# Performance work log

Measured on AMD Instinct MI355X. Metric: run time of the kernel, lower is better.

The kernel has to match this reference:

```python
import jax, jax.numpy as jnp
import numpy as np

N, D, E, K, L, NF, VOCAB = 100000, 128, 600000, 3, 3, 9, 100
BN_EPS = 1e-5
S = 0.05


def setup_inputs() -> dict:
    key = jax.random.key(0)
    ks = jax.random.split(key, 8)
    return {
        "x": jax.random.randint(ks[0], (N, NF), 0, VOCAB),
        "k_edges": jax.random.randint(ks[1], (K, 2, E), 0, N),
        "emb_tables": jax.random.normal(ks[2], (NF, VOCAB, D), jnp.float32) * S,
        "W1": jax.random.normal(ks[3], (L, D, 2 * D), jnp.float32) * S,
        "b1": jnp.zeros((L, 2 * D), jnp.float32),
        "g1": jnp.ones((L, 2 * D), jnp.float32),
        "be1": jnp.zeros((L, 2 * D), jnp.float32),
        "W2": jax.random.normal(ks[4], (L, 2 * D, D), jnp.float32) * S,
        "b2": jnp.zeros((L, D), jnp.float32),
        "eps": jnp.zeros((L,), jnp.float32),
        "alpha": jnp.zeros((L, K), jnp.float32),
        "bn_g": jnp.ones((L, D), jnp.float32),
        "bn_b": jnp.zeros((L, D), jnp.float32),
    }


def _bn(h, g, b):
    # training-mode BatchNorm1d over the node (batch) axis
    mu = h.mean(axis=0)
    var = h.var(axis=0)
    return (h - mu) * jax.lax.rsqrt(var + BN_EPS) * g + b


def _gin(h, src, dst, eps_l, W1_l, b1_l, g1_l, be1_l, W2_l, b2_l):
    # NodeGINConv (train_eps): mlp((1+eps)*x + sum_{j->i} x_j)
    agg = jax.ops.segment_sum(h[src], dst, num_segments=N)  # [N, D]
    z = (1.0 + eps_l) * h + agg
    z = jax.nn.relu(_bn(z @ W1_l + b1_l, g1_l, be1_l))  # [N, 2D]
    return z @ W2_l + b2_l  # [N, D]


def reference(x, k_edges, emb_tables, W1, b1, g1, be1, W2, b2, eps, alpha, bn_g, bn_b):
    # AtomEncoder: sum of per-feature embedding lookups -> [N, D]
    h = jnp.take_along_axis(
        emb_tables.transpose(1, 0, 2),  # [VOCAB, NF, D]
        x.T[..., None].transpose(1, 0, 2) * 0 + 0,  # placeholder avoided below
        axis=0,
    ) if False else emb_tables[jnp.arange(NF)[None, :], x].sum(axis=1)
    for l in range(L):
        # one shared wrapped GIN conv applied to each of the K relational edge sets
        msgs = jax.vmap(
            lambda e: _gin(h, e[0], e[1], eps[l], W1[l], b1[l], g1[l], be1[l], W2[l], b2[l])
        )(k_edges)  # [K, N, D]
        a = jax.nn.softmax(alpha[l])  # [K]
        h = jnp.einsum('knd,k->nd', msgs, a)
        h = jax.nn.relu(_bn(h, bn_g[l], bn_b[l]))  # dropout p=0 / eval -> identity
    return h
```

## Files before the change

### kernel.cpp

```cpp
#include <hip/hip_runtime.h>

#define NV     100000
#define DD     128
#define D2     256
#define EE     600000
#define KK     3
#define LL     3
#define NFEAT  9
#define VOCABS 100

#define NBKT   196
#define BCAP   8192

typedef __attribute__((ext_vector_type(8))) short short8;
typedef __attribute__((ext_vector_type(4))) float f32x4;
typedef __attribute__((ext_vector_type(4))) unsigned int uint4v;

#define PA      0
#define PA2     8
#define PB2     136
#define PA1K(k) (264 + (k)*512)
#define PB1K(k) (264 + (k)*512 + 256)

#define ZS(k)  ((k)*512)
#define ZQ(k)  ((k)*512 + 256)
#define HSUM   1536
#define HSQ    1664

#define HB_OFF   ((size_t)0)
#define ZIN_OFF  ((size_t)25600000)
#define HNB_OFF  ((size_t)102400000)
#define O_BASE   ((size_t)128000000)

__device__ __forceinline__ unsigned short f2bf(float f) {
    union { float f; unsigned int u; } v; v.f = f;
    return (unsigned short)((v.u + 0x7FFFu + ((v.u >> 16) & 1u)) >> 16);
}
__device__ __forceinline__ float bf2f(unsigned short u) {
    union { unsigned int u; float f; } v; v.u = ((unsigned int)u) << 16;
    return v.f;
}

__global__ void k_embed(const int* __restrict__ x, const float* __restrict__ emb,
                        unsigned short* __restrict__ hb) {
    int id = blockIdx.x*256 + threadIdx.x;
    int n = id >> 5, q = id & 31;
    if (n >= NV) return;
    const int* xr = x + n*NFEAT;
    f32x4 acc = {0.f,0.f,0.f,0.f};
    #pragma unroll
    for (int f = 0; f < NFEAT; ++f) {
        int idx = xr[f];
        acc += *(const f32x4*)(emb + ((size_t)(f*VOCABS + idx)*DD + q*4));
    }
    unsigned short pk[4];
    pk[0] = f2bf(acc[0]); pk[1] = f2bf(acc[1]); pk[2] = f2bf(acc[2]); pk[3] = f2bf(acc[3]);
    *(unsigned long long*)(hb + (size_t)n*DD + q*4) = *(unsigned long long*)pk;
}

__global__ void kA_bin(const int* __restrict__ ke, int* __restrict__ cursor,
                       uint2* __restrict__ pairs) {
    __shared__ int hist[NBKT], excl[NBKT], ofs[NBKT], gbase[NBKT];
    __shared__ int sc[256];
    __shared__ uint2 buf[4096];
    const int rel = blockIdx.y, t = threadIdx.x;
    const int e0 = blockIdx.x * 4096;
    const int cnt = min(4096, EE - e0);
    const int* srcA = ke + (size_t)(rel*2)*EE + e0;
    const int* dstA = ke + (size_t)(rel*2+1)*EE + e0;
    if (t < NBKT) hist[t] = 0;
    __syncthreads();
    for (int i = t; i < cnt; i += 256) atomicAdd(&hist[dstA[i] >> 9], 1);
    __syncthreads();
    const int hv = (t < NBKT) ? hist[t] : 0;
    sc[t] = hv;
    for (int off = 1; off < 256; off <<= 1) {
        __syncthreads();
        int v = (t >= off) ? sc[t-off] : 0;
        __syncthreads();
        sc[t] += v;
    }
    __syncthreads();
    if (t < NBKT) {
        excl[t] = sc[t] - hv;
        ofs[t]  = sc[t] - hv;
        if (hv > 0) gbase[t] = atomicAdd(&cursor[rel*NBKT + t], hv);
    }
    __syncthreads();
    for (int i = t; i < cnt; i += 256) {
        unsigned int s = (unsigned int)srcA[i], d = (unsigned int)dstA[i];
        int p = atomicAdd(&ofs[d >> 9], 1);
        uint2 u; u.x = s; u.y = d;
        buf[p] = u;
    }
    __syncthreads();
    for (int i = t; i < cnt; i += 256) {
        uint2 u = buf[i];
        int b = (int)(u.y >> 9);
        int pos = gbase[b] + (i - excl[b]);
        if (pos < BCAP) pairs[(size_t)(rel*NBKT + b)*BCAP + pos] = u;
    }
}

__global__ void kB_scan(const int* __restrict__ cursor, int* __restrict__ ebase) {
    __shared__ int sc[256];
    const int t = threadIdx.x;
    for (int rel = 0; rel < KK; ++rel) {
        int hv = (t < NBKT) ? min(cursor[rel*NBKT + t], BCAP) : 0;
        sc[t] = hv;
        for (int off = 1; off < 256; off <<= 1) {
            __syncthreads();
            int v = (t >= off) ? sc[t-off] : 0;
            __syncthreads();
            sc[t] += v;
        }
        __syncthreads();
        if (t < NBKT) ebase[rel*NBKT + t] = sc[t] - hv;
        __syncthreads();
    }
}

__global__ void kB_fill(const uint2* __restrict__ pairs, const int* __restrict__ cursor,
                        const int* __restrict__ ebase, int* __restrict__ rp,
                        int* __restrict__ col) {
    __shared__ int h2[512], excl[512], cur[512], sc[256];
    const int b = blockIdx.x, rel = blockIdx.y, t = threadIdx.x;
    const int lo = b * 512;
    const int cnt = min(cursor[rel*NBKT + b], BCAP);
    const int base = ebase[rel*NBKT + b];
    const uint2* P = pairs + (size_t)(rel*NBKT + b)*BCAP;
    h2[t] = 0; h2[t+256] = 0; cur[t] = 0; cur[t+256] = 0;
    __syncthreads();
    for (int i = t; i < cnt; i += 256) atomicAdd(&h2[(int)P[i].y - lo], 1);
    __syncthreads();
    const int a0 = h2[2*t], a1 = h2[2*t+1];
    sc[t] = a0 + a1;
    for (int off = 1; off < 256; off <<= 1) {
        __syncthreads();
        int v = (t >= off) ? sc[t-off] : 0;
        __syncthreads();
        sc[t] += v;
    }
    __syncthreads();
    const int e2 = sc[t] - (a0 + a1);
    excl[2*t] = e2; excl[2*t+1] = e2 + a0;
    __syncthreads();
    for (int tt = t; tt < 512; tt += 256) {
        int n = lo + tt;
        if (n <= NV) rp[(size_t)rel*(NV+1) + n] = base + excl[tt];
    }
    for (int i = t; i < cnt; i += 256) {
        uint2 u = P[i];
        int r = (int)u.y - lo;
        int p = atomicAdd(&cur[r], 1);
        col[(size_t)rel*EE + base + excl[r] + p] = (int)u.x;
    }
}

__global__ void k_prep(const float* __restrict__ W1, const float* __restrict__ W2,
                       const float* __restrict__ alpha, const int l,
                       unsigned short* __restrict__ w1f, unsigned short* __restrict__ w2f,
                       float* __restrict__ params) {
    int id = blockIdx.x*256 + threadIdx.x;
    if (id == 0) {
        float a0 = alpha[l*KK+0], a1 = alpha[l*KK+1], a2 = alpha[l*KK+2];
        float m = fmaxf(a0, fmaxf(a1, a2));
        float e0 = expf(a0-m), e1 = expf(a1-m), e2 = expf(a2-m);
        float inv = 1.f/(e0+e1+e2);
        params[PA+0] = e0*inv; params[PA+1] = e1*inv; params[PA+2] = e2*inv;
    }
    if (id < 4096) {
        int kt = id >> 10, nt = (id >> 6) & 15, lane = id & 63;
        int r = lane & 15, g = lane >> 4;
        const float* Wl = W1 + (size_t)l*DD*D2;
        #pragma unroll
        for (int e = 0; e < 8; ++e) {
            int kk = kt*32 + g*8 + e, c = nt*16 + r;
            w1f[(size_t)id*8 + e] = f2bf(Wl[(size_t)kk*D2 + c]);
        }
    } else if (id < 8192) {
        int id2 = id - 4096;
        int kt = id2 >> 9, nt = (id2 >> 6) & 7, lane = id2 & 63;
        int r = lane & 15, g = lane >> 4;
        const float* Wl = W2 + (size_t)l*D2*DD;
        #pragma unroll
        for (int e = 0; e < 8; ++e) {
            int kk = kt*32 + g*8 + e, c = nt*16 + r;
            w2f[(size_t)id2*8 + e] = f2bf(Wl[(size_t)kk*DD + c]);
        }
    }
}

__global__ void k_gather3(const unsigned short* __restrict__ hb, const int* __restrict__ rp,
                          const int* __restrict__ col, const float* __restrict__ epsp,
                          unsigned short* __restrict__ zin) {
    int gid = blockIdx.x*256 + threadIdx.x;
    int n = gid >> 6;
    if (n >= NV) return;
    const int lane = threadIdx.x & 63;
    const int q = lane >> 4, r = lane & 15;
    const uint4v* h4 = (const uint4v*)hb;
    const float epsv = 1.0f + epsp[0];
    const uint4v sv = h4[(size_t)n*16 + r];
    int b0[KK], dg[KK], cv[KK];
    #pragma unroll
    for (int k = 0; k < KK; ++k) {
        const int* rpk = rp + (size_t)k*(NV+1) + n;
        int a = rpk[0], b = rpk[1];
        b0[k] = a; dg[k] = b - a;
        cv[k] = (lane < dg[k]) ? col[(size_t)k*EE + a + lane] : 0;
    }
    float acc[KK][8];
    #pragma unroll
    for (int k = 0; k < KK; ++k)
        #pragma unroll
        for (int i = 0; i < 8; ++i) acc[k][i] = 0.0f;
    #pragma unroll
    for (int k = 0; k < KK; ++k) {
        const int dc = min(dg[k], 64);
        for (int base = 0; base < dc; base += 8) {
            const int e0 = base + q;
            const int e1 = base + q + 4;
            int s0 = __shfl(cv[k], e0);
            int s1 = __shfl(cv[k], e1);
            uint4v v0 = h4[(size_t)s0*16 + r];
            uint4v v1 = h4[(size_t)s1*16 + r];
            if (e0 < dc) {
                #pragma unroll
                for (int c = 0; c < 4; ++c) {
                    acc[k][2*c]   += bf2f((unsigned short)(v0[c] & 0xFFFFu));
                    acc[k][2*c+1] += bf2f((unsigned short)(v0[c] >> 16));
                }
            }
            if (e1 < dc) {
                #pragma unroll
                for (int c = 0; c < 4; ++c) {
                    acc[k][2*c]   += bf2f((unsigned short)(v1[c] & 0xFFFFu));
                    acc[k][2*c+1] += bf2f((unsigned short)(v1[c] >> 16));
                }
            }
        }
        for (int j = b0[k] + 64 + q; j < b0[k] + dg[k]; j += 4) {
            int s0 = col[(size_t)k*EE + j];
            uint4v v0 = h4[(size_t)s0*16 + r];
            #pragma unroll
            for (int c = 0; c < 4; ++c) {
                acc[k][2*c]   += bf2f((unsigned short)(v0[c] & 0xFFFFu));
                acc[k][2*c+1] += bf2f((unsigned short)(v0[c] >> 16));
            }
        }
    }
    #pragma unroll
    for (int k = 0; k < KK; ++k) {
        #pragma unroll
        for (int i = 0; i < 8; ++i) {
            acc[k][i] += __shfl_xor(acc[k][i], 16);
            acc[k][i] += __shfl_xor(acc[k][i], 32);
        }
        if (q == 0) {
            uint4v pk;
            #pragma unroll
            for (int c = 0; c < 4; ++c) {
                float lo = acc[k][2*c]   + epsv * bf2f((unsigned short)(sv[c] & 0xFFFFu));
                float hi = acc[k][2*c+1] + epsv * bf2f((unsigned short)(sv[c] >> 16));
                pk[c] = (unsigned int)f2bf(lo) | ((unsigned int)f2bf(hi) << 16);
            }
            ((uint4v*)(zin + (size_t)k*NV*DD))[(size_t)n*16 + r] = pk;
        }
    }
}

__launch_bounds__(256, 2)
__global__ void k_stats3(const unsigned short* __restrict__ zin,
                         const unsigned short* __restrict__ w1f,
                         float* __restrict__ stats) {
    __shared__ __align__(16) unsigned short bfr1[32768];
    __shared__ float scf[1024];
    const int t = threadIdx.x;
    const int krel = blockIdx.y;
    const unsigned short* zk = zin + (size_t)krel*NV*DD;
    float* zsum = stats + ZS(krel);
    float* zsq  = stats + ZQ(krel);
    for (int i = t; i < 4096; i += 256)
        *(uint4v*)(bfr1 + i*8) = *(const uint4v*)(w1f + i*8);
    const int lane = t & 63, w = t >> 6;
    const int r_ = lane & 15, g = lane >> 4;
    const int rt = w & 1, ch = w >> 1;
    __syncthreads();
    float ssum[8] = {0,0,0,0,0,0,0,0};
    float ssq[8]  = {0,0,0,0,0,0,0,0};
    for (int tile = blockIdx.x; tile < NV/32; tile += gridDim.x) {
        const int row0 = tile*32;
        short8 af[4];
        #pragma unroll
        for (int kt = 0; kt < 4; ++kt)
            af[kt] = *(const short8*)(zk + (size_t)(row0 + rt*16 + r_)*DD + kt*32 + g*8);
        #pragma unroll
        for (int ct = 0; ct < 8; ++ct) {
            const int ntg = ch*8 + ct;
            f32x4 c = {0.f,0.f,0.f,0.f};
            #pragma unroll
            for (int kt = 0; kt < 4; ++kt) {
                short8 b = *(const short8*)(bfr1 + ((size_t)((kt*16 + ntg)*64 + lane))*8);
                c = __builtin_amdgcn_mfma_f32_16x16x32_bf16(af[kt], b, c, 0, 0, 0);
            }
            float s = c[0]+c[1]+c[2]+c[3];
            float q = c[0]*c[0]+c[1]*c[1]+c[2]*c[2]+c[3]*c[3];
            s += __shfl_xor(s, 16); q += __shfl_xor(q, 16);
            s += __shfl_xor(s, 32); q += __shfl_xor(q, 32);
            ssum[ct] += s; ssq[ct] += q;
        }
    }
    if (g == 0) {
        #pragma unroll
        for (int ct = 0; ct < 8; ++ct) {
            const int colc = (ch*8 + ct)*16 + r_;
            scf[rt*256 + colc]       = ssum[ct];
            scf[512 + rt*256 + colc] = ssq[ct];
        }
    }
    __syncthreads();
    atomicAdd(zsum + t, scf[t]       + scf[256 + t]);
    atomicAdd(zsq  + t, scf[512 + t] + scf[768 + t]);
}

__global__ void k_bnprep3(float* __restrict__ stats,
                          const float* __restrict__ g1l, const float* __restrict__ be1l,
                          float* __restrict__ params) {
    int j = threadIdx.x;
    #pragma unroll
    for (int k = 0; k < KK; ++k) {
        float ak  = params[PA + k];
        float mu  = stats[ZS(k) + j] * (1.0f/NV);
        float var = stats[ZQ(k) + j] * (1.0f/NV) - mu*mu;
        float A = g1l[j] * rsqrtf(var + 1e-5f);
        params[PA1K(k) + j] = ak * A;
        params[PB1K(k) + j] = ak * (be1l[j] - mu*A);
        stats[ZS(k) + j] = 0.0f; stats[ZQ(k) + j] = 0.0f;
    }
}

#define LOAD_AF(AF, TILE) {                                                        \
    const int rowp_ = (TILE)*32;                                                   \
    _Pragma("unroll")                                                              \
    for (int k = 0; k < KK; ++k) {                                                 \
        _Pragma("unroll")                                                          \
        for (int kt = 0; kt < 4; ++kt)                                             \
            AF[k][kt] = *(const short8*)(zin + (size_t)k*NV*DD                     \
                          + (size_t)(rowp_ + rt*16 + r_)*DD + kt*32 + g*8);        \
    }                                                                              \
}

#define GBODY(AF, AFN) {                                                           \
    const int cur_ = tile, nx_ = tile + step;                                      \
    f32x4 y[4];                                                                    \
    _Pragma("unroll")                                                              \
    for (int ct = 0; ct < 4; ++ct) y[ct] = (f32x4){0.f,0.f,0.f,0.f};               \
    _Pragma("unroll")                                                              \
    for (int k = 0; k < KK; ++k) {                                                 \
        _Pragma("unroll")                                                          \
        for (int ct = 0; ct < 4; ++ct) {                                           \
            const int ntg = ch*4 + ct;                                             \
            f32x4 c = {0.f,0.f,0.f,0.f};                                           \
            _Pragma("unroll")                                                      \
            for (int kt = 0; kt < 4; ++kt) {                                       \
                short8 b = *(const short8*)(bfr1 + ((size_t)((kt*16 + ntg)*64 + lane))*8); \
                c = __builtin_amdgcn_mfma_f32_16x16x32_bf16(AF[k][kt], b, c, 0, 0, 0); \
            }                                                                      \
            _Pragma("unroll")                                                      \
            for (int reg = 0; reg < 4; ++reg)                                      \
                y[ct][reg] += fmaxf(pa1[k][ct]*c[reg] + pb1[k][ct], 0.0f);         \
        }                                                                          \
    }                                                                              \
    if (nx_ < NT) LOAD_AF(AFN, nx_);                                               \
    __syncthreads();                                                               \
    _Pragma("unroll")                                                              \
    for (int ct = 0; ct < 4; ++ct) {                                               \
        const int col2 = ((ch*4 + ct)*16 + r_)*2;                                  \
        _Pragma("unroll")                                                          \
        for (int reg = 0; reg < 4; ++reg) {                                        \
            const int row = rt*16 + g*4 + reg;                                     \
            *(unsigned short*)(yt + row*512 + (col2 ^ ((row & 15) << 4))) = f2bf(y[ct][reg]); \
        }                                                                          \
    }                                                                              \
    __syncthreads();                                                               \
    short8 ya[8];                                                                  \
    _Pragma("unroll")                                                              \
    for (int kt = 0; kt < 8; ++kt)                                                 \
        ya[kt] = *(const short8*)(yt + arow*512 + ((kt*64 + g*16) ^ ((arow & 15) << 4))); \
    _Pragma("unroll")                                                              \
    for (int ct2 = 0; ct2 < 2; ++ct2) {                                            \
        const int ntg2 = ch*2 + ct2;                                               \
        f32x4 c = {0.f,0.f,0.f,0.f};                                               \
        _Pragma("unroll")                                                          \
        for (int kt = 0; kt < 8; ++kt) {                                           \
            short8 b = *(const short8*)(bfr2 + ((size_t)((kt*8 + ntg2)*64 + lane))*8); \
            c = __builtin_amdgcn_mfma_f32_16x16x32_bf16(ya[kt], b, c, 0, 0, 0);    \
        }                                                                          \
        unsigned short* hp = hnb + (size_t)(cur_*32 + rt*16 + g*4)*DD + ntg2*16 + r_; \
        float ps = 0.0f, pq = 0.0f;                                                \
        _Pragma("unroll")                                                          \
        for (int reg = 0; reg < 4; ++reg) {                                        \
            float xv = c[reg];                                                     \
            hp[(size_t)reg*DD] = f2bf(xv);                                         \
            ps += xv; pq += xv*xv;                                                 \
        }                                                                          \
        ps += __shfl_xor(ps, 16); pq += __shfl_xor(pq, 16);                        \
        ps += __shfl_xor(ps, 32); pq += __shfl_xor(pq, 32);                        \
        ssum[ct2] += ps; ssq[ct2] += pq;                                           \
    }                                                                              \
    tile = nx_;                                                                    \
}

__launch_bounds__(512, 2)
__global__ void k_gemm2f(const unsigned short* __restrict__ zin,
                         const unsigned short* __restrict__ w1f,
                         const unsigned short* __restrict__ w2f,
                         const float* __restrict__ params,
                         unsigned short* __restrict__ hnb,
                         float* __restrict__ hsum, float* __restrict__ hsq) {
    __shared__ __align__(16) unsigned short bfr1[32768];
    __shared__ __align__(16) unsigned short bfr2[32768];
    __shared__ __align__(16) unsigned char yt[16384];
    const int t = threadIdx.x;
    for (int i = t; i < 4096; i += 512)
        *(uint4v*)(bfr1 + i*8) = *(const uint4v*)(w1f + i*8);
    for (int i = t; i < 4096; i += 512)
        *(uint4v*)(bfr2 + i*8) = *(const uint4v*)(w2f + i*8);
    const int lane = t & 63, w = t >> 6;
    const int r_ = lane & 15, g = lane >> 4;
    const int rt = w & 1, ch = w >> 1;
    const int arow = rt*16 + r_;
    float pa1[KK][4], pb1[KK][4];
    #pragma unroll
    for (int k = 0; k < KK; ++k) {
        #pragma unroll
        for (int ct = 0; ct < 4; ++ct) {
            const int colc = (ch*4 + ct)*16 + r_;
            pa1[k][ct] = params[PA1K(k) + colc];
            pb1[k][ct] = params[PB1K(k) + colc];
        }
    }
    __syncthreads();
    float ssum[2] = {0,0}, ssq[2] = {0,0};
    const int NT = NV/32;
    const int step = gridDim.x;
    int tile = blockIdx.x;
    short8 afA[KK][4], afB[KK][4];
    LOAD_AF(afA, tile);
    while (tile < NT) {
        GBODY(afA, afB);
        if (tile >= NT) break;
        GBODY(afB, afA);
    }
    __syncthreads();
    float* scf = (float*)yt;
    if (g == 0) {
        #pragma unroll
        for (int ct2 = 0; ct2 < 2; ++ct2) {
            scf[w*32 + ct2*16 + r_]       = ssum[ct2];
            scf[256 + w*32 + ct2*16 + r_] = ssq[ct2];
        }
    }
    __syncthreads();
    if (t < 128) {
        const int chc = t >> 5, idx = t & 31;
        float s = 0.0f, q = 0.0f;
        #pragma unroll
        for (int rr = 0; rr < 2; ++rr) {
            s += scf[(chc*2 + rr)*32 + idx];
            q += scf[256 + (chc*2 + rr)*32 + idx];
        }
        atomicAdd(hsum + t, s);
        atomicAdd(hsq + t, q);
    }
}

__global__ void k_bnprep2(float* __restrict__ hsum, float* __restrict__ hsq,
                          const float* __restrict__ bng, const float* __restrict__ bnb,
                          float* __restrict__ params) {
    int j = threadIdx.x;
    float mu  = hsum[j] * (1.0f/NV);
    float var = hsq[j]  * (1.0f/NV) - mu*mu;
    float A = bng[j] * rsqrtf(var + 1e-5f);
    params[PA2 + j] = A;
    params[PB2 + j] = bnb[j] - mu*A;
    hsum[j] = 0.0f; hsq[j] = 0.0f;
}

__global__ void k_bnapply_mid(const unsigned short* __restrict__ hnb,
                              const float* __restrict__ params,
                              unsigned short* __restrict__ hb) {
    int id = blockIdx.x*256 + threadIdx.x;
    const int col0 = (id & 15)*8;
    short8 v = *(const short8*)(hnb + (size_t)id*8);
    f32x4 A0 = *(const f32x4*)(params + PA2 + col0);
    f32x4 A1 = *(const f32x4*)(params + PA2 + col0 + 4);
    f32x4 B0 = *(const f32x4*)(params + PB2 + col0);
    f32x4 B1 = *(const f32x4*)(params + PB2 + col0 + 4);
    short8 o;
    #pragma unroll
    for (int j = 0; j < 4; ++j) {
        o[j]   = (short)f2bf(fmaxf(A0[j]*bf2f((unsigned short)v[j])   + B0[j], 0.0f));
        o[j+4] = (short)f2bf(fmaxf(A1[j]*bf2f((unsigned short)v[j+4]) + B1[j], 0.0f));
    }
    *(short8*)(hb + (size_t)id*8) = o;
}

__global__ void k_bnapply_fin(const unsigned short* __restrict__ hnb,
                              const float* __restrict__ params,
                              float* __restrict__ out) {
    int id = blockIdx.x*256 + threadIdx.x;
    const int col0 = (id & 15)*8;
    short8 v = *(const short8*)(hnb + (size_t)id*8);
    f32x4 A0 = *(const f32x4*)(params + PA2 + col0);
    f32x4 A1 = *(const f32x4*)(params + PA2 + col0 + 4);
    f32x4 B0 = *(const f32x4*)(params + PB2 + col0);
    f32x4 B1 = *(const f32x4*)(params + PB2 + col0 + 4);
    f32x4 o0, o1;
    #pragma unroll
    for (int j = 0; j < 4; ++j) {
        o0[j] = fmaxf(A0[j]*bf2f((unsigned short)v[j])   + B0[j], 0.0f);
        o1[j] = fmaxf(A1[j]*bf2f((unsigned short)v[j+4]) + B1[j], 0.0f);
    }
    *(f32x4*)(out + (size_t)id*8)     = o0;
    *(f32x4*)(out + (size_t)id*8 + 4) = o1;
}

extern "C" void kernel_launch(void* const* d_in, const int* in_sizes, int n_in,
                              void* d_out, int out_size, void* d_ws, size_t ws_size,
                              hipStream_t stream) {
    const int*   x     = (const int*)d_in[0];
    const int*   ke    = (const int*)d_in[1];
    const float* emb   = (const float*)d_in[2];
    const float* W1    = (const float*)d_in[3];
    const float* g1    = (const float*)d_in[5];
    const float* be1   = (const float*)d_in[6];
    const float* W2    = (const float*)d_in[7];
    const float* eps   = (const float*)d_in[9];
    const float* alpha = (const float*)d_in[10];
    const float* bng   = (const float*)d_in[11];
    const float* bnb   = (const float*)d_in[12];

    char* ws = (char*)d_ws;
    unsigned short* hb     = (unsigned short*)(ws + HB_OFF);
    unsigned short* zin    = (unsigned short*)(ws + ZIN_OFF);
    unsigned short* hnb    = (unsigned short*)(ws + HNB_OFF);
    size_t o = O_BASE;
    unsigned short* w1f    = (unsigned short*)(ws + o);          o += 65536;
    unsigned short* w2f    = (unsigned short*)(ws + o);          o += 65536;
    float*          stats  = (float*)(ws + o);                   o += 8192;
    float*          params = (float*)(ws + o);                   o += 8192;
    int*            rp     = (int*)(ws + o);                     o += 1200128;
    int*            col    = (int*)(ws + o);                     o += 7200000;
    int*            cur    = (int*)(ws + o);                     o += 4096;
    int*            ebase  = (int*)(ws + o);                     o += 4096;
    uint2*          pairs  = (uint2*)(ws + ZIN_OFF);

    k_embed<<<12500, 256, 0, stream>>>(x, emb, hb);

    hipMemsetAsync(cur, 0, KK*NBKT*sizeof(int), stream);
    hipMemsetAsync(stats, 0, 8192, stream);
    kA_bin<<<dim3(147, KK), 256, 0, stream>>>(ke, cur, pairs);
    kB_scan<<<1, 256, 0, stream>>>(cur, ebase);
    kB_fill<<<dim3(NBKT, KK), 256, 0, stream>>>(pairs, cur, ebase, rp, col);

    for (int l = 0; l < LL; ++l) {
        k_prep<<<32, 256, 0, stream>>>(W1, W2, alpha, l, w1f, w2f, params);
        k_gather3<<<25000, 256, 0, stream>>>(hb, rp, col, eps + l, zin);
        k_stats3<<<dim3(512, KK), 256, 0, stream>>>(zin, w1f, stats);
        k_bnprep3<<<1, 256, 0, stream>>>(stats, g1 + l*D2, be1 + l*D2, params);
        k_gemm2f<<<256, 512, 0, stream>>>(zin, w1f, w2f, params, hnb,
                                          stats + HSUM, stats + HSQ);
        k_bnprep2<<<1, 128, 0, stream>>>(stats + HSUM, stats + HSQ,
                                         bng + l*DD, bnb + l*DD, params);
        if (l < LL-1) k_bnapply_mid<<<6250, 256, 0, stream>>>(hnb, params, hb);
        else          k_bnapply_fin<<<6250, 256, 0, stream>>>(hnb, params, (float*)d_out);
    }
}
```

Measured before the change: 720.9 us.

## Use zero sentinel row to drop gather bounds checks and double-buffer GEMM LDS

A zeroed padding row is added past the last node in the bf16 feature buffer, and out-of-range neighbor slots now point at it. This lets the gather loop drop its per-edge validity branches and accumulate unconditionally with packed bf16 unpacking and a hardware pack-convert instruction. The fused GEMM kernel ping-pongs between two LDS staging buffers, which removes one __syncthreads per tile. The cost is extra loads of the sentinel row for low-degree nodes, more workspace, and higher LDS use per block.

```diff
diff --git a/kernel.cpp b/kernel.cpp
--- a/kernel.cpp
+++ b/kernel.cpp
@@ -14,6 +14,7 @@
 
 typedef __attribute__((ext_vector_type(8))) short short8;
 typedef __attribute__((ext_vector_type(4))) float f32x4;
+typedef __attribute__((ext_vector_type(2))) float f32x2;
 typedef __attribute__((ext_vector_type(4))) unsigned int uint4v;
 
 #define PA      0
@@ -28,9 +29,9 @@
 #define HSQ    1664
 
 #define HB_OFF   ((size_t)0)
-#define ZIN_OFF  ((size_t)25600000)
-#define HNB_OFF  ((size_t)102400000)
-#define O_BASE   ((size_t)128000000)
+#define ZIN_OFF  ((size_t)25700000)
+#define HNB_OFF  ((size_t)102500000)
+#define O_BASE   ((size_t)128100000)
 
 __device__ __forceinline__ unsigned short f2bf(float f) {
     union { float f; unsigned int u; } v; v.f = f;
@@ -39,13 +40,22 @@
 __device__ __forceinline__ float bf2f(unsigned short u) {
     union { unsigned int u; float f; } v; v.u = ((unsigned int)u) << 16;
     return v.f;
+}
+__device__ __forceinline__ f32x2 up2(unsigned int v) {
+    union { unsigned int u[2]; f32x2 f; } w;
+    w.u[0] = v << 16;
+    w.u[1] = v & 0xFFFF0000u;
+    return w.f;
 }
 
 __global__ void k_embed(const int* __restrict__ x, const float* __restrict__ emb,
                         unsigned short* __restrict__ hb) {
     int id = blockIdx.x*256 + threadIdx.x;
     int n = id >> 5, q = id & 31;
-    if (n >= NV) return;
+    if (n >= NV) {
+        if (n < NV + 8) *(unsigned long long*)(hb + (size_t)n*DD + q*4) = 0ull;
+        return;
+    }
     const int* xr = x + n*NFEAT;
     f32x4 acc = {0.f,0.f,0.f,0.f};
     #pragma unroll
@@ -195,77 +205,73 @@
                           const int* __restrict__ col, const float* __restrict__ epsp,
                           unsigned short* __restrict__ zin) {
     int gid = blockIdx.x*256 + threadIdx.x;
-    int n = gid >> 6;
-    if (n >= NV) return;
+    int n0 = gid >> 6;
+    if (n0 >= NV) return;
+    const int n = __builtin_amdgcn_readfirstlane(n0);
     const int lane = threadIdx.x & 63;
     const int q = lane >> 4, r = lane & 15;
-    const uint4v* h4 = (const uint4v*)hb;
+    const int r16 = r << 4;
+    const char* hbase = (const char*)hb;
     const float epsv = 1.0f + epsp[0];
-    const uint4v sv = h4[(size_t)n*16 + r];
+    const uint4v sv = *(const uint4v*)(hbase + (((unsigned)n << 8) + r16));
     int b0[KK], dg[KK], cv[KK];
     #pragma unroll
     for (int k = 0; k < KK; ++k) {
-        const int* rpk = rp + (size_t)k*(NV+1) + n;
-        int a = rpk[0], b = rpk[1];
+        int a = rp[k*(NV+1) + n];
+        int b = rp[k*(NV+1) + n + 1];
         b0[k] = a; dg[k] = b - a;
-        cv[k] = (lane < dg[k]) ? col[(size_t)k*EE + a + lane] : 0;
-    }
-    float acc[KK][8];
+        cv[k] = (lane < dg[k]) ? col[(size_t)k*EE + a + lane] : NV;
+    }
+    f32x2 acc[KK][4];
     #pragma unroll
     for (int k = 0; k < KK; ++k)
         #pragma unroll
-        for (int i = 0; i < 8; ++i) acc[k][i] = 0.0f;
+        for (int c = 0; c < 4; ++c) acc[k][c] = (f32x2){0.f, 0.f};
     #pragma unroll
     for (int k = 0; k < KK; ++k) {
         const int dc = min(dg[k], 64);
         for (int base = 0; base < dc; base += 8) {
-            const int e0 = base + q;
-            const int e1 = base + q + 4;
-            int s0 = __shfl(cv[k], e0);
-            int s1 = __shfl(cv[k], e1);
-            uint4v v0 = h4[(size_t)s0*16 + r];
-            uint4v v1 = h4[(size_t)s1*16 + r];
-            if (e0 < dc) {
-                #pragma unroll
-                for (int c = 0; c < 4; ++c) {
-                    acc[k][2*c]   += bf2f((unsigned short)(v0[c] & 0xFFFFu));
-                    acc[k][2*c+1] += bf2f((unsigned short)(v0[c] >> 16));
-                }
-            }
-            if (e1 < dc) {
-                #pragma unroll
-                for (int c = 0; c < 4; ++c) {
-                    acc[k][2*c]   += bf2f((unsigned short)(v1[c] & 0xFFFFu));
-                    acc[k][2*c+1] += bf2f((unsigned short)(v1[c] >> 16));
-                }
+            int s0 = __shfl(cv[k], base + q);
+            int s1 = __shfl(cv[k], base + q + 4);
+            uint4v v0 = *(const uint4v*)(hbase + (((unsigned)s0 << 8) + r16));
+            uint4v v1 = *(const uint4v*)(hbase + (((unsigned)s1 << 8) + r16));
+            #pragma unroll
+            for (int c = 0; c < 4; ++c) {
+                acc[k][c] += up2(v0[c]);
+                acc[k][c] += up2(v1[c]);
             }
         }
         for (int j = b0[k] + 64 + q; j < b0[k] + dg[k]; j += 4) {
             int s0 = col[(size_t)k*EE + j];
-            uint4v v0 = h4[(size_t)s0*16 + r];
+            uint4v v0 = *(const uint4v*)(hbase + (((unsigned)s0 << 8) + r16));
             #pragma unroll
-            for (int c = 0; c < 4; ++c) {
-                acc[k][2*c]   += bf2f((unsigned short)(v0[c] & 0xFFFFu));
-                acc[k][2*c+1] += bf2f((unsigned short)(v0[c] >> 16));
-            }
+            for (int c = 0; c < 4; ++c) acc[k][c] += up2(v0[c]);
         }
     }
     #pragma unroll
     for (int k = 0; k < KK; ++k) {
         #pragma unroll
-        for (int i = 0; i < 8; ++i) {
-            acc[k][i] += __shfl_xor(acc[k][i], 16);
-            acc[k][i] += __shfl_xor(acc[k][i], 32);
-        }
-        if (q == 0) {
+        for (int c = 0; c < 4; ++c) {
+            acc[k][c][0] += __shfl_xor(acc[k][c][0], 16);
+            acc[k][c][1] += __shfl_xor(acc[k][c][1], 16);
+            acc[k][c][0] += __shfl_xor(acc[k][c][0], 32);
+            acc[k][c][1] += __shfl_xor(acc[k][c][1], 32);
+        }
+    }
+    if (q == 0) {
+        #pragma unroll
+        for (int k = 0; k < KK; ++k) {
             uint4v pk;
             #pragma unroll
             for (int c = 0; c < 4; ++c) {
-                float lo = acc[k][2*c]   + epsv * bf2f((unsigned short)(sv[c] & 0xFFFFu));
-                float hi = acc[k][2*c+1] + epsv * bf2f((unsigned short)(sv[c] >> 16));
-                pk[c] = (unsigned int)f2bf(lo) | ((unsigned int)f2bf(hi) << 16);
+                f32x2 s2 = up2(sv[c]);
+                float lo = acc[k][c][0] + epsv * s2[0];
+                float hi = acc[k][c][1] + epsv * s2[1];
+                unsigned int pko;
+                asm("v_cvt_pk_bf16_f32 %0, %1, %2" : "=v"(pko) : "v"(lo), "v"(hi));
+                pk[c] = pko;
             }
-            ((uint4v*)(zin + (size_t)k*NV*DD))[(size_t)n*16 + r] = pk;
+            *(uint4v*)((char*)zin + (size_t)k*NV*DD*2 + (((unsigned)n << 8) + r16)) = pk;
         }
     }
 }
@@ -351,7 +357,7 @@
     }                                                                              \
 }
 
-#define GBODY(AF, AFN) {                                                           \
+#define GBODY(AF, AFN, YT) {                                                       \
     const int cur_ = tile, nx_ = tile + step;                                      \
     f32x4 y[4];                                                                    \
     _Pragma("unroll")                                                              \
@@ -373,21 +379,20 @@
         }                                                                          \
     }                                                                              \
     if (nx_ < NT) LOAD_AF(AFN, nx_);                                               \
-    __syncthreads();                                                               \
     _Pragma("unroll")                                                              \
     for (int ct = 0; ct < 4; ++ct) {                                               \
         const int col2 = ((ch*4 + ct)*16 + r_)*2;                                  \
         _Pragma("unroll")                                                          \
         for (int reg = 0; reg < 4; ++reg) {                                        \
             const int row = rt*16 + g*4 + reg;                                     \
-            *(unsigned short*)(yt + row*512 + (col2 ^ ((row & 15) << 4))) = f2bf(y[ct][reg]); \
+            *(unsigned short*)(YT + row*512 + (col2 ^ ((row & 15) << 4))) = f2bf(y[ct][reg]); \
         }                                                                          \
     }                                                                              \
     __syncthreads();                                                               \
     short8 ya[8];                                                                  \
     _Pragma("unroll")                                                              \
     for (int kt = 0; kt < 8; ++kt)                                                 \
-        ya[kt] = *(const short8*)(yt + arow*512 + ((kt*64 + g*16) ^ ((arow & 15) << 4))); \
+        ya[kt] = *(const short8*)(YT + arow*512 + ((kt*64 + g*16) ^ ((arow & 15) << 4))); \
     _Pragma("unroll")                                                              \
     for (int ct2 = 0; ct2 < 2; ++ct2) {                                            \
         const int ntg2 = ch*2 + ct2;                                               \
@@ -421,7 +426,8 @@
                          float* __restrict__ hsum, float* __restrict__ hsq) {
     __shared__ __align__(16) unsigned short bfr1[32768];
     __shared__ __align__(16) unsigned short bfr2[32768];
-    __shared__ __align__(16) unsigned char yt[16384];
+    __shared__ __align__(16) unsigned char ytA[16384];
+    __shared__ __align__(16) unsigned char ytB[16384];
     const int t = threadIdx.x;
     for (int i = t; i < 4096; i += 512)
         *(uint4v*)(bfr1 + i*8) = *(const uint4v*)(w1f + i*8);
@@ -449,12 +455,12 @@
     short8 afA[KK][4], afB[KK][4];
     LOAD_AF(afA, tile);
     while (tile < NT) {
-        GBODY(afA, afB);
+        GBODY(afA, afB, ytA);
         if (tile >= NT) break;
-        GBODY(afB, afA);
-    }
-    __syncthreads();
-    float* scf = (float*)yt;
+        GBODY(afB, afA, ytB);
+    }
+    __syncthreads();
+    float* scf = (float*)ytA;
     if (g == 0) {
         #pragma unroll
         for (int ct2 = 0; ct2 < 2; ++ct2) {
@@ -557,7 +563,7 @@
     int*            ebase  = (int*)(ws + o);                     o += 4096;
     uint2*          pairs  = (uint2*)(ws + ZIN_OFF);
 
-    k_embed<<<12500, 256, 0, stream>>>(x, emb, hb);
+    k_embed<<<12501, 256, 0, stream>>>(x, emb, hb);
 
     hipMemsetAsync(cur, 0, KK*NBKT*sizeof(int), stream);
     hipMemsetAsync(stats, 0, 8192, stream);
```

Result: slower. 784.2 us (+8.8%).
